# Performance work log

Hardware: AMD Instinct MI355X
Metric: run time of the kernel (lower is better)

The kernel has to match this reference:

```python
import jax, jax.numpy as jnp
import numpy as np

N_FREQ = 48  # tcnn Frequency encoding n_frequencies


def _freq_encode(x):
    # x: [N,3] in [0,1]; tcnn Frequency: sin/cos of x * 2^f * pi, f=0..F-1
    freqs = (2.0 ** jnp.arange(N_FREQ, dtype=jnp.float32)) * jnp.pi  # [F]
    ang = x[:, :, None] * freqs  # [N,3,F]
    enc = jnp.stack([jnp.sin(ang), jnp.cos(ang)], axis=-1)  # [N,3,F,2]
    return enc.reshape(x.shape[0], -1)  # [N, 3*F*2]


def _bilinear_sample(plane, coords):
    # plane: [R,R,F] (H,W,feat); coords: [N,2] in [-1,1], coords[:,0]->width(x), coords[:,1]->height(y)
    # matches torch grid_sample(align_corners=True, bilinear) for in-range coords
    R = plane.shape[0]
    gx = (coords[:, 0] + 1.0) * 0.5 * (R - 1)
    gy = (coords[:, 1] + 1.0) * 0.5 * (R - 1)
    x0f = jnp.clip(jnp.floor(gx), 0.0, R - 1)
    y0f = jnp.clip(jnp.floor(gy), 0.0, R - 1)
    x0 = x0f.astype(jnp.int32)
    y0 = y0f.astype(jnp.int32)
    x1 = jnp.minimum(x0 + 1, R - 1)
    y1 = jnp.minimum(y0 + 1, R - 1)
    wx = (gx - x0f)[:, None]
    wy = (gy - y0f)[:, None]
    v00 = plane[y0, x0]
    v01 = plane[y0, x1]
    v10 = plane[y1, x0]
    v11 = plane[y1, x1]
    return (v00 * (1 - wx) * (1 - wy) + v01 * wx * (1 - wy)
            + v10 * (1 - wx) * wy + v11 * wx * wy)  # [N,F]


def setup_inputs() -> dict:
    key = jax.random.key(0)
    ks = jax.random.split(key, 8)
    N = 524288
    res, fdim = 32, 16
    enc_dim = 3 * N_FREQ * 2  # 288
    d_in = enc_dim + fdim     # 304
    h = 64
    positions = jax.random.uniform(ks[0], (N, 3), dtype=jnp.float32)
    aabb = jnp.array([0.0, 0.0, 0.0, 1.0, 1.0, 1.0], dtype=jnp.float32)
    triplane = jax.random.normal(ks[1], (3, res, res, fdim), dtype=jnp.float32) * 0.001
    W0 = jax.random.normal(ks[2], (d_in, h), dtype=jnp.float32) / np.sqrt(d_in)
    W1 = jax.random.normal(ks[3], (h, h), dtype=jnp.float32) / np.sqrt(h)
    W2 = jax.random.normal(ks[4], (h, h), dtype=jnp.float32) / np.sqrt(h)
    W3 = jax.random.normal(ks[5], (h, 4), dtype=jnp.float32) / np.sqrt(h)
    return {"positions": positions, "aabb": aabb, "triplane": triplane,
            "W0": W0, "W1": W1, "W2": W2, "W3": W3}


def reference(positions, aabb, triplane, W0, W1, W2, W3):
    aabb_min, aabb_max = aabb[:3], aabb[3:]
    xn = (positions - aabb_min) / (aabb_max - aabb_min)          # normalized [0,1]
    sc = 2.0 * xn - 1.0                                          # scaled_coords in [-1,1]
    selector = jnp.all((xn > 0.0) & (xn < 1.0), axis=-1)
    # plane coordinate pairs as in the torch code
    coords = jnp.stack([
        jnp.stack([sc[:, 0], sc[:, 1]], axis=1),  # xy
        jnp.stack([sc[:, 0], sc[:, 2]], axis=1),  # xz
        jnp.stack([sc[:, 1], sc[:, 2]], axis=1),  # zy
    ], axis=0)  # [3,N,2]
    feats = jax.vmap(_bilinear_sample)(triplane, coords).sum(0)  # [N,fdim]
    h = jnp.concatenate([_freq_encode(xn), feats], axis=1)       # [N,304]
    h = jnp.sin(h @ W0)
    h = jnp.sin(h @ W1)
    h = jnp.sin(h @ W2)
    out = h @ W3                                                 # [N,4]
    rgb = jax.nn.sigmoid(out[:, :3])
    density = jnp.exp(out[:, 3:4] - 1.0) * selector[:, None]     # trunc_exp(x-1)
    return rgb, density
```

## Files before the change

kernel.cpp:

```cpp
#include <hip/hip_runtime.h>
#include <stdint.h>

typedef _Float16 half8  __attribute__((ext_vector_type(8)));
typedef _Float16 half2v __attribute__((ext_vector_type(2)));
typedef float f32x4 __attribute__((ext_vector_type(4)));

#define TPW 8
#define WPB 8
#define NT  512
#define W0S 304

__device__ __forceinline__ half2v pkrtz(float a, float b) {
    return __builtin_bit_cast(half2v, __builtin_amdgcn_cvt_pkrtz(a, b));
}

static __device__ __forceinline__ void wave_fence() {
    __builtin_amdgcn_wave_barrier();
    asm volatile("" ::: "memory");
}

__device__ __forceinline__ float bf2f(uint16_t u) {
    return __uint_as_float(((uint32_t)u) << 16);
}
__device__ __forceinline__ uint16_t f2bf(float f) {
    uint32_t u = __float_as_uint(f);
    u = (u + 0x7FFFu + ((u >> 16) & 1u)) >> 16;
    return (uint16_t)u;
}

template<bool BF>
__device__ __forceinline__ float lde(const void* p, uint32_t i) {
    if constexpr (BF) return bf2f(((const uint16_t*)p)[i]);
    else              return ((const float*)p)[i];
}
template<bool BF>
__device__ __forceinline__ void st1(void* p, uint32_t i, float v) {
    if constexpr (BF) ((uint16_t*)p)[i] = f2bf(v);
    else              ((float*)p)[i] = v;
}
template<bool BF>
__device__ __forceinline__ void ld8(const void* p, uint32_t i, float* o) {
    if constexpr (BF) {
        const uint4 c = *(const uint4*)((const uint16_t*)p + i);
        const uint32_t* pu = (const uint32_t*)&c;
#pragma unroll
        for (int j = 0; j < 4; ++j) {
            o[2 * j]     = __uint_as_float(pu[j] << 16);
            o[2 * j + 1] = __uint_as_float(pu[j] & 0xFFFF0000u);
        }
    } else {
        const float4 a = *(const float4*)((const float*)p + i);
        const float4 b = *(const float4*)((const float*)p + i + 4);
        o[0] = a.x; o[1] = a.y; o[2] = a.z; o[3] = a.w;
        o[4] = b.x; o[5] = b.y; o[6] = b.z; o[7] = b.w;
    }
}

__device__ __forceinline__ int hswz(int p, int g) {
    return p * 72 + ((g + 2 * (p >> 2)) & 7) * 8;
}

template<bool BF>
__device__ __forceinline__ void run_all(
    const void* __restrict__ posg, const void* __restrict__ aabbg,
    const void* __restrict__ tpg,
    const void* __restrict__ w0g, const void* __restrict__ w1g,
    const void* __restrict__ w2g, const void* __restrict__ w3g,
    void* __restrict__ outp, int npts,
    _Float16* w0t, _Float16* w1t, _Float16* w2t, _Float16* w3t, _Float16* hbuf)
{
    const int tid = threadIdx.x;
    const float I2PI = 0.15915494309189535f;

    for (int e = tid; e < 16; e += NT) w0t[64 * W0S + e] = (_Float16)0.0f;
    for (int e = tid; e < 304 * 64; e += NT) { int k = e >> 6, n = e & 63; w0t[n * W0S + k] = (_Float16)(lde<BF>(w0g, e) * I2PI); }
    for (int e = tid; e < 64 * 64;  e += NT) { int k = e >> 6, n = e & 63; w1t[n * 72 + k] = (_Float16)(lde<BF>(w1g, e) * I2PI);
                                               w2t[n * 72 + k] = (_Float16)(lde<BF>(w2g, e) * I2PI); }
    for (int e = tid; e < 64 * 4;   e += NT) { int k = e >> 2, n = e & 3;  w3t[n * 72 + k] = (_Float16)lde<BF>(w3g, e); }
    __syncthreads();

    const int w = tid >> 6, lane = tid & 63;
    const int m = lane & 15, q = lane >> 4;
    _Float16* hb = hbuf + w * (16 * 72);

    const float mn0 = lde<BF>(aabbg, 0), mn1 = lde<BF>(aabbg, 1), mn2 = lde<BF>(aabbg, 2);
    const float mx0 = lde<BF>(aabbg, 3), mx1 = lde<BF>(aabbg, 4), mx2 = lde<BF>(aabbg, 5);

    const double IH = 0x1.45f306dc9c883p-2;
    const double IL = -0x1.6b01ec5417056p-56;
    const float PIF  = 3.14159274101257324f;
    const f32x4 z4 = {0.f, 0.f, 0.f, 0.f};

    const int tile0 = (blockIdx.x * WPB + w) * TPW;

    float cp0, cp1, cp2;
    {
        const int pt = tile0 * 16 + m;
        cp0 = lde<BF>(posg, 3 * pt + 0);
        cp1 = lde<BF>(posg, 3 * pt + 1);
        cp2 = lde<BF>(posg, 3 * pt + 2);
    }

    for (int it = 0; it < TPW; ++it) {
        const int base = (tile0 + it) * 16;
        const float p0 = cp0, p1 = cp1, p2 = cp2;
        {
            const int nit = (it + 1 < TPW) ? it + 1 : it;
            const int pt2 = (tile0 + nit) * 16 + m;
            cp0 = lde<BF>(posg, 3 * pt2 + 0);
            cp1 = lde<BF>(posg, 3 * pt2 + 1);
            cp2 = lde<BF>(posg, 3 * pt2 + 2);
        }

        float xn[3];
        xn[0] = (p0 - mn0) / (mx0 - mn0);
        xn[1] = (p1 - mn1) / (mx1 - mn1);
        xn[2] = (p2 - mn2) / (mx2 - mn2);

        const bool sel = xn[0] > 0.f && xn[0] < 1.f && xn[1] > 0.f && xn[1] < 1.f
                      && xn[2] > 0.f && xn[2] < 1.f;
        const unsigned long long bm = __ballot(sel);

        double wh[3], wl[3];
#pragma unroll
        for (int d = 0; d < 3; ++d) {
            const float mf = xn[d] * PIF;
            const double md = (double)mf;
            const double hi = md * IH;
            const double r  = __builtin_fma(md, IH, -hi);
            wh[d] = hi;
            wl[d] = __builtin_fma(md, IL, r);
        }

        float fe[8];
#pragma unroll
        for (int j = 0; j < 8; ++j) fe[j] = 0.f;
        if (q < 2) {
            const int fo = q * 8;
            float g[3];
#pragma unroll
            for (int d = 0; d < 3; ++d) g[d] = xn[d] * 31.f;
            float v[8];
#pragma unroll
            for (int p = 0; p < 3; ++p) {
                const float gx = (p == 2) ? g[1] : g[0];
                const float gy = (p == 0) ? g[1] : g[2];
                const float x0f = fminf(fmaxf(floorf(gx), 0.f), 31.f);
                const float y0f = fminf(fmaxf(floorf(gy), 0.f), 31.f);
                const int x0 = (int)x0f, y0 = (int)y0f;
                int x1 = x0 + 1; if (x1 > 31) x1 = 31;
                int y1 = y0 + 1; if (y1 > 31) y1 = 31;
                const float wx = gx - x0f, wy = gy - y0f;
                const float w00 = (1.f - wx) * (1.f - wy);
                const float w01 = wx * (1.f - wy);
                const float w10 = (1.f - wx) * wy;
                const float w11 = wx * wy;
                const uint32_t pb = p * 16384 + fo;
                ld8<BF>(tpg, pb + y0 * 512 + x0 * 16, v);
#pragma unroll
                for (int j = 0; j < 8; ++j) fe[j] += v[j] * w00;
                ld8<BF>(tpg, pb + y0 * 512 + x1 * 16, v);
#pragma unroll
                for (int j = 0; j < 8; ++j) fe[j] += v[j] * w01;
                ld8<BF>(tpg, pb + y1 * 512 + x0 * 16, v);
#pragma unroll
                for (int j = 0; j < 8; ++j) fe[j] += v[j] * w10;
                ld8<BF>(tpg, pb + y1 * 512 + x1 * 16, v);
#pragma unroll
                for (int j = 0; j < 8; ++j) fe[j] += v[j] * w11;
            }
        }

        f32x4 acc[4] = {z4, z4, z4, z4};
#pragma unroll
        for (int d = 0; d < 3; ++d) {
#pragma unroll
            for (int cc = 0; cc < 3; ++cc) {
                const int e0 = 16 * cc + 4 * q - 1;
                const double zp = __builtin_bit_cast(double, (uint64_t)(1023 + e0) << 52);
                const double z  = wh[d] * zp;
                const double zl = wl[d] * zp;
                const double fr = z - __builtin_floor(z);
                const float t = (float)(fr + zl);
                float s = __builtin_amdgcn_sinf(t);
                float c = __builtin_amdgcn_cosf(t);
                union { half8 h8; half2v h2[4]; } au;
                au.h2[0] = pkrtz(s, c);
#pragma unroll
                for (int jj = 1; jj < 4; ++jj) {
                    const float t2 = s + s;
                    const float sn = t2 * c;
                    c = __builtin_fmaf(-t2, s, 1.0f);
                    s = sn;
                    au.h2[jj] = pkrtz(s, c);
                }
                const int ch = 3 * d + cc;
#pragma unroll
                for (int t4 = 0; t4 < 4; ++t4) {
                    const half8 b = *(const half8*)&w0t[(t4 * 16 + m) * W0S + ch * 32 + q * 8];
                    acc[t4] = __builtin_amdgcn_mfma_f32_16x16x32_f16(au.h8, b, acc[t4], 0, 0, 0);
                }
            }
        }
        {
            union { half8 h8; half2v h2[4]; } au;
            if (q < 2) {
#pragma unroll
                for (int i = 0; i < 4; ++i)
                    au.h2[i] = pkrtz(fe[2 * i], fe[2 * i + 1]);
            } else {
#pragma unroll
                for (int j = 0; j < 8; ++j) au.h8[j] = (_Float16)0.f;
            }
#pragma unroll
            for (int t4 = 0; t4 < 4; ++t4) {
                const half8 b = *(const half8*)&w0t[(t4 * 16 + m) * W0S + 288 + q * 8];
                acc[t4] = __builtin_amdgcn_mfma_f32_16x16x32_f16(au.h8, b, acc[t4], 0, 0, 0);
            }
        }

#pragma unroll
        for (int t4 = 0; t4 < 4; ++t4) {
            const int gw = 2 * t4 + (m >> 3);
#pragma unroll
            for (int rg = 0; rg < 4; ++rg)
                hb[hswz(4 * q + rg, gw) + (m & 7)] =
                    (_Float16)__builtin_amdgcn_sinf(acc[t4][rg]);
        }
        wave_fence();

        f32x4 acc2[4] = {z4, z4, z4, z4};
#pragma unroll
        for (int c = 0; c < 2; ++c) {
            const half8 a = *(const half8*)&hb[hswz(m, 4 * c + q)];
#pragma unroll
            for (int t4 = 0; t4 < 4; ++t4) {
                const half8 b = *(const half8*)&w1t[(t4 * 16 + m) * 72 + c * 32 + q * 8];
                acc2[t4] = __builtin_amdgcn_mfma_f32_16x16x32_f16(a, b, acc2[t4], 0, 0, 0);
            }
        }
        wave_fence();
#pragma unroll
        for (int t4 = 0; t4 < 4; ++t4) {
            const int gw = 2 * t4 + (m >> 3);
#pragma unroll
            for (int rg = 0; rg < 4; ++rg)
                hb[hswz(4 * q + rg, gw) + (m & 7)] =
                    (_Float16)__builtin_amdgcn_sinf(acc2[t4][rg]);
        }
        wave_fence();

        f32x4 accx[4] = {z4, z4, z4, z4};
#pragma unroll
        for (int c = 0; c < 2; ++c) {
            const half8 a = *(const half8*)&hb[hswz(m, 4 * c + q)];
#pragma unroll
            for (int t4 = 0; t4 < 4; ++t4) {
                const half8 b = *(const half8*)&w2t[(t4 * 16 + m) * 72 + c * 32 + q * 8];
                accx[t4] = __builtin_amdgcn_mfma_f32_16x16x32_f16(a, b, accx[t4], 0, 0, 0);
            }
        }
        wave_fence();
#pragma unroll
        for (int t4 = 0; t4 < 4; ++t4) {
            const int gw = 2 * t4 + (m >> 3);
#pragma unroll
            for (int rg = 0; rg < 4; ++rg)
                hb[hswz(4 * q + rg, gw) + (m & 7)] =
                    (_Float16)__builtin_amdgcn_sinf(accx[t4][rg]);
        }
        wave_fence();

        f32x4 acc3 = z4;
#pragma unroll
        for (int c = 0; c < 2; ++c) {
            const half8 a = *(const half8*)&hb[hswz(m, 4 * c + q)];
            const half8 b = *(const half8*)&w3t[(m & 3) * 72 + c * 32 + q * 8];
            acc3 = __builtin_amdgcn_mfma_f32_16x16x32_f16(a, b, acc3, 0, 0, 0);
        }
        wave_fence();

        if (m < 3) {
#pragma unroll
            for (int rg = 0; rg < 4; ++rg) {
                const float s = 1.f / (1.f + __expf(-acc3[rg]));
                st1<BF>(outp, (uint32_t)(base + 4 * q + rg) * 3u + m, s);
            }
        } else if (m == 3) {
            float dv[4];
#pragma unroll
            for (int rg = 0; rg < 4; ++rg) {
                float dens = __expf(acc3[rg] - 1.f);
                if (!((bm >> (4 * q + rg)) & 1ull)) dens = 0.f;
                dv[rg] = dens;
            }
            const uint32_t di = 3u * (uint32_t)npts + (uint32_t)(base + 4 * q);
            if constexpr (BF) {
                ushort4 pk;
                pk.x = f2bf(dv[0]); pk.y = f2bf(dv[1]);
                pk.z = f2bf(dv[2]); pk.w = f2bf(dv[3]);
                *(ushort4*)((uint16_t*)outp + di) = pk;
            } else {
                float4 pk = {dv[0], dv[1], dv[2], dv[3]};
                *(float4*)((float*)outp + di) = pk;
            }
        }
    }
}

__global__ __launch_bounds__(NT, 2)
void tri_mlp(const void* __restrict__ posg, const void* __restrict__ aabbg,
             const void* __restrict__ tpg,
             const void* __restrict__ w0g, const void* __restrict__ w1g,
             const void* __restrict__ w2g, const void* __restrict__ w3g,
             void* __restrict__ outp, int npts)
{
    __shared__ alignas(16) _Float16 w0t[64 * W0S + 16];
    __shared__ alignas(16) _Float16 w1t[64 * 72];
    __shared__ alignas(16) _Float16 w2t[64 * 72];
    __shared__ alignas(16) _Float16 w3t[4 * 72];
    __shared__ alignas(16) _Float16 hbuf[WPB * 16 * 72];

    const bool bf = (((const uint32_t*)aabbg)[2] != 0u);
    if (bf) run_all<true >(posg, aabbg, tpg, w0g, w1g, w2g, w3g, outp, npts, w0t, w1t, w2t, w3t, hbuf);
    else    run_all<false>(posg, aabbg, tpg, w0g, w1g, w2g, w3g, outp, npts, w0t, w1t, w2t, w3t, hbuf);
}

extern "C" void kernel_launch(void* const* d_in, const int* in_sizes, int n_in,
                              void* d_out, int out_size, void* d_ws, size_t ws_size,
                              hipStream_t stream) {
    const int npts = in_sizes[0] / 3;
    const int blocks = npts / (16 * WPB * TPW);
    tri_mlp<<<blocks, NT, 0, stream>>>(d_in[0], d_in[1], d_in[2], d_in[3],
                                       d_in[4], d_in[5], d_in[6], d_out, npts);
}
```

Measured before the change: 146.3 us.

## Swap MFMA operand roles and pass hidden activations via ds_bpermute instead of LDS

Transposes the MLP GEMMs so weights feed the A operand and activations the B operand, making each lane's accumulator hold a point's outputs. Hidden activations between layers are then re-laid out with cross-lane ds_bpermute shuffles instead of a per-wave LDS round trip with wave barriers, and the hbuf shared buffer is removed. This cuts LDS stores, loads and fences per layer and lowers shared memory use. The output stage now writes per point from q==0 lanes using the local selector instead of a ballot. In exchange it adds bpermute traffic and some register pressure.

New measurement: 280.9 us. +91.9%, slower.

```diff
diff --git a/kernel.cpp b/kernel.cpp
--- a/kernel.cpp
+++ b/kernel.cpp
@@ -12,11 +12,6 @@
 
 __device__ __forceinline__ half2v pkrtz(float a, float b) {
     return __builtin_bit_cast(half2v, __builtin_amdgcn_cvt_pkrtz(a, b));
-}
-
-static __device__ __forceinline__ void wave_fence() {
-    __builtin_amdgcn_wave_barrier();
-    asm volatile("" ::: "memory");
 }
 
 __device__ __forceinline__ float bf2f(uint16_t u) {
@@ -56,8 +51,30 @@
     }
 }
 
-__device__ __forceinline__ int hswz(int p, int g) {
-    return p * 72 + ((g + 2 * (p >> 2)) & 7) * 8;
+__device__ __forceinline__ void sin_shuffle(const f32x4* acc, int addr0, bool hi,
+                                            half8* b0, half8* b1) {
+    uint32_t P[8];
+#pragma unroll
+    for (int t4 = 0; t4 < 4; ++t4) {
+        const float s0 = __builtin_amdgcn_sinf(acc[t4][0]);
+        const float s1 = __builtin_amdgcn_sinf(acc[t4][1]);
+        const float s2 = __builtin_amdgcn_sinf(acc[t4][2]);
+        const float s3 = __builtin_amdgcn_sinf(acc[t4][3]);
+        P[2 * t4]     = __builtin_bit_cast(uint32_t, pkrtz(s0, s1));
+        P[2 * t4 + 1] = __builtin_bit_cast(uint32_t, pkrtz(s2, s3));
+    }
+    union { uint32_t d[4]; half8 h8; } u0, u1;
+#pragma unroll
+    for (int c = 0; c < 2; ++c) {
+#pragma unroll
+        for (int jd = 0; jd < 4; ++jd) {
+            const int ad = addr0 + (jd >> 1) * 64;
+            const uint32_t lo = (uint32_t)__builtin_amdgcn_ds_bpermute(ad, (int)P[4 * c + (jd & 1)]);
+            const uint32_t hv = (uint32_t)__builtin_amdgcn_ds_bpermute(ad, (int)P[4 * c + 2 + (jd & 1)]);
+            (c ? u1.d : u0.d)[jd] = hi ? hv : lo;
+        }
+    }
+    *b0 = u0.h8; *b1 = u1.h8;
 }
 
 template<bool BF>
@@ -67,7 +84,7 @@
     const void* __restrict__ w0g, const void* __restrict__ w1g,
     const void* __restrict__ w2g, const void* __restrict__ w3g,
     void* __restrict__ outp, int npts,
-    _Float16* w0t, _Float16* w1t, _Float16* w2t, _Float16* w3t, _Float16* hbuf)
+    _Float16* w0t, _Float16* w1t, _Float16* w2t, _Float16* w3t)
 {
     const int tid = threadIdx.x;
     const float I2PI = 0.15915494309189535f;
@@ -81,7 +98,8 @@
 
     const int w = tid >> 6, lane = tid & 63;
     const int m = lane & 15, q = lane >> 4;
-    _Float16* hb = hbuf + w * (16 * 72);
+    const int addr0 = (m + 32 * (q & 1)) * 4;
+    const bool hi = (q >> 1) != 0;
 
     const float mn0 = lde<BF>(aabbg, 0), mn1 = lde<BF>(aabbg, 1), mn2 = lde<BF>(aabbg, 2);
     const float mx0 = lde<BF>(aabbg, 3), mx1 = lde<BF>(aabbg, 4), mx2 = lde<BF>(aabbg, 5);
@@ -119,16 +137,15 @@
 
         const bool sel = xn[0] > 0.f && xn[0] < 1.f && xn[1] > 0.f && xn[1] < 1.f
                       && xn[2] > 0.f && xn[2] < 1.f;
-        const unsigned long long bm = __ballot(sel);
 
         double wh[3], wl[3];
 #pragma unroll
         for (int d = 0; d < 3; ++d) {
             const float mf = xn[d] * PIF;
             const double md = (double)mf;
-            const double hi = md * IH;
-            const double r  = __builtin_fma(md, IH, -hi);
-            wh[d] = hi;
+            const double hid = md * IH;
+            const double r  = __builtin_fma(md, IH, -hid);
+            wh[d] = hid;
             wl[d] = __builtin_fma(md, IL, r);
         }
 
@@ -197,8 +214,8 @@
                 const int ch = 3 * d + cc;
 #pragma unroll
                 for (int t4 = 0; t4 < 4; ++t4) {
-                    const half8 b = *(const half8*)&w0t[(t4 * 16 + m) * W0S + ch * 32 + q * 8];
-                    acc[t4] = __builtin_amdgcn_mfma_f32_16x16x32_f16(au.h8, b, acc[t4], 0, 0, 0);
+                    const half8 aw = *(const half8*)&w0t[(t4 * 16 + m) * W0S + ch * 32 + q * 8];
+                    acc[t4] = __builtin_amdgcn_mfma_f32_16x16x32_f16(aw, au.h8, acc[t4], 0, 0, 0);
                 }
             }
         }
@@ -214,96 +231,54 @@
             }
 #pragma unroll
             for (int t4 = 0; t4 < 4; ++t4) {
-                const half8 b = *(const half8*)&w0t[(t4 * 16 + m) * W0S + 288 + q * 8];
-                acc[t4] = __builtin_amdgcn_mfma_f32_16x16x32_f16(au.h8, b, acc[t4], 0, 0, 0);
-            }
-        }
-
-#pragma unroll
-        for (int t4 = 0; t4 < 4; ++t4) {
-            const int gw = 2 * t4 + (m >> 3);
-#pragma unroll
-            for (int rg = 0; rg < 4; ++rg)
-                hb[hswz(4 * q + rg, gw) + (m & 7)] =
-                    (_Float16)__builtin_amdgcn_sinf(acc[t4][rg]);
-        }
-        wave_fence();
-
+                const half8 aw = *(const half8*)&w0t[(t4 * 16 + m) * W0S + 288 + q * 8];
+                acc[t4] = __builtin_amdgcn_mfma_f32_16x16x32_f16(aw, au.h8, acc[t4], 0, 0, 0);
+            }
+        }
+
+        half8 hb0, hb1;
+        sin_shuffle(acc, addr0, hi, &hb0, &hb1);
         f32x4 acc2[4] = {z4, z4, z4, z4};
 #pragma unroll
         for (int c = 0; c < 2; ++c) {
-            const half8 a = *(const half8*)&hb[hswz(m, 4 * c + q)];
+            const half8 bfr = c ? hb1 : hb0;
 #pragma unroll
             for (int t4 = 0; t4 < 4; ++t4) {
-                const half8 b = *(const half8*)&w1t[(t4 * 16 + m) * 72 + c * 32 + q * 8];
-                acc2[t4] = __builtin_amdgcn_mfma_f32_16x16x32_f16(a, b, acc2[t4], 0, 0, 0);
-            }
-        }
-        wave_fence();
-#pragma unroll
-        for (int t4 = 0; t4 < 4; ++t4) {
-            const int gw = 2 * t4 + (m >> 3);
-#pragma unroll
-            for (int rg = 0; rg < 4; ++rg)
-                hb[hswz(4 * q + rg, gw) + (m & 7)] =
-                    (_Float16)__builtin_amdgcn_sinf(acc2[t4][rg]);
-        }
-        wave_fence();
-
+                const half8 aw = *(const half8*)&w1t[(t4 * 16 + m) * 72 + c * 32 + q * 8];
+                acc2[t4] = __builtin_amdgcn_mfma_f32_16x16x32_f16(aw, bfr, acc2[t4], 0, 0, 0);
+            }
+        }
+
+        sin_shuffle(acc2, addr0, hi, &hb0, &hb1);
         f32x4 accx[4] = {z4, z4, z4, z4};
 #pragma unroll
         for (int c = 0; c < 2; ++c) {
-            const half8 a = *(const half8*)&hb[hswz(m, 4 * c + q)];
+            const half8 bfr = c ? hb1 : hb0;
 #pragma unroll
             for (int t4 = 0; t4 < 4; ++t4) {
-                const half8 b = *(const half8*)&w2t[(t4 * 16 + m) * 72 + c * 32 + q * 8];
-                accx[t4] = __builtin_amdgcn_mfma_f32_16x16x32_f16(a, b, accx[t4], 0, 0, 0);
-            }
-        }
-        wave_fence();
-#pragma unroll
-        for (int t4 = 0; t4 < 4; ++t4) {
-            const int gw = 2 * t4 + (m >> 3);
-#pragma unroll
-            for (int rg = 0; rg < 4; ++rg)
-                hb[hswz(4 * q + rg, gw) + (m & 7)] =
-                    (_Float16)__builtin_amdgcn_sinf(accx[t4][rg]);
-        }
-        wave_fence();
-
+                const half8 aw = *(const half8*)&w2t[(t4 * 16 + m) * 72 + c * 32 + q * 8];
+                accx[t4] = __builtin_amdgcn_mfma_f32_16x16x32_f16(aw, bfr, accx[t4], 0, 0, 0);
+            }
+        }
+
+        sin_shuffle(accx, addr0, hi, &hb0, &hb1);
         f32x4 acc3 = z4;
 #pragma unroll
         for (int c = 0; c < 2; ++c) {
-            const half8 a = *(const half8*)&hb[hswz(m, 4 * c + q)];
-            const half8 b = *(const half8*)&w3t[(m & 3) * 72 + c * 32 + q * 8];
-            acc3 = __builtin_amdgcn_mfma_f32_16x16x32_f16(a, b, acc3, 0, 0, 0);
-        }
-        wave_fence();
-
-        if (m < 3) {
-#pragma unroll
-            for (int rg = 0; rg < 4; ++rg) {
-                const float s = 1.f / (1.f + __expf(-acc3[rg]));
-                st1<BF>(outp, (uint32_t)(base + 4 * q + rg) * 3u + m, s);
-            }
-        } else if (m == 3) {
-            float dv[4];
-#pragma unroll
-            for (int rg = 0; rg < 4; ++rg) {
-                float dens = __expf(acc3[rg] - 1.f);
-                if (!((bm >> (4 * q + rg)) & 1ull)) dens = 0.f;
-                dv[rg] = dens;
-            }
-            const uint32_t di = 3u * (uint32_t)npts + (uint32_t)(base + 4 * q);
-            if constexpr (BF) {
-                ushort4 pk;
-                pk.x = f2bf(dv[0]); pk.y = f2bf(dv[1]);
-                pk.z = f2bf(dv[2]); pk.w = f2bf(dv[3]);
-                *(ushort4*)((uint16_t*)outp + di) = pk;
-            } else {
-                float4 pk = {dv[0], dv[1], dv[2], dv[3]};
-                *(float4*)((float*)outp + di) = pk;
-            }
+            const half8 bfr = c ? hb1 : hb0;
+            const half8 aw = *(const half8*)&w3t[(m & 3) * 72 + c * 32 + q * 8];
+            acc3 = __builtin_amdgcn_mfma_f32_16x16x32_f16(aw, bfr, acc3, 0, 0, 0);
+        }
+
+        if (q == 0) {
+#pragma unroll
+            for (int c = 0; c < 3; ++c) {
+                const float s = 1.f / (1.f + __expf(-acc3[c]));
+                st1<BF>(outp, (uint32_t)(base + m) * 3u + c, s);
+            }
+            float dens = __expf(acc3[3] - 1.f);
+            if (!sel) dens = 0.f;
+            st1<BF>(outp, 3u * (uint32_t)npts + (uint32_t)(base + m), dens);
         }
     }
 }
@@ -319,11 +294,10 @@
     __shared__ alignas(16) _Float16 w1t[64 * 72];
     __shared__ alignas(16) _Float16 w2t[64 * 72];
     __shared__ alignas(16) _Float16 w3t[4 * 72];
-    __shared__ alignas(16) _Float16 hbuf[WPB * 16 * 72];
 
     const bool bf = (((const uint32_t*)aabbg)[2] != 0u);
-    if (bf) run_all<true >(posg, aabbg, tpg, w0g, w1g, w2g, w3g, outp, npts, w0t, w1t, w2t, w3t, hbuf);
-    else    run_all<false>(posg, aabbg, tpg, w0g, w1g, w2g, w3g, outp, npts, w0t, w1t, w2t, w3t, hbuf);
+    if (bf) run_all<true >(posg, aabbg, tpg, w0g, w1g, w2g, w3g, outp, npts, w0t, w1t, w2t, w3t);
+    else    run_all<false>(posg, aabbg, tpg, w0g, w1g, w2g, w3g, outp, npts, w0t, w1t, w2t, w3t);
 }
 
 extern "C" void kernel_launch(void* const* d_in, const int* in_sizes, int n_in,
```

## Process two 16-point tiles per iteration to interleave MFMA chains

Applied to the files above, without the earlier changes.

Each wave now handles two tiles per loop iteration. The encoding, triplane sampling and first-layer MFMAs for both tiles are interleaved so the two independent accumulator chains can hide MFMA latency, and the weight-fragment LDS reads are shared between the tiles. The hidden layers are staggered per tile through the single per-wave scratch buffer. The wave_barrier builtin is dropped and only a compiler memory fence is kept. This roughly doubles accumulator register pressure, which could cause spills or lower occupancy at launch bounds (512,2), and leaves LDS ordering within the wave resting on the compiler fence alone.

Measured after the change: 150.2 us. 2.6% more time.

```diff
diff --git a/kernel.cpp b/kernel.cpp
--- a/kernel.cpp
+++ b/kernel.cpp
@@ -14,8 +14,7 @@
     return __builtin_bit_cast(half2v, __builtin_amdgcn_cvt_pkrtz(a, b));
 }
 
-static __device__ __forceinline__ void wave_fence() {
-    __builtin_amdgcn_wave_barrier();
+static __device__ __forceinline__ void mem_fence() {
     asm volatile("" ::: "memory");
 }
 
@@ -93,216 +92,230 @@
 
     const int tile0 = (blockIdx.x * WPB + w) * TPW;
 
-    float cp0, cp1, cp2;
-    {
-        const int pt = tile0 * 16 + m;
-        cp0 = lde<BF>(posg, 3 * pt + 0);
-        cp1 = lde<BF>(posg, 3 * pt + 1);
-        cp2 = lde<BF>(posg, 3 * pt + 2);
+    auto xpose_sin = [&](const f32x4* a4) {
+#pragma unroll
+        for (int t4 = 0; t4 < 4; ++t4) {
+            const int gw = 2 * t4 + (m >> 3);
+#pragma unroll
+            for (int rg = 0; rg < 4; ++rg)
+                hb[hswz(4 * q + rg, gw) + (m & 7)] =
+                    (_Float16)__builtin_amdgcn_sinf(a4[t4][rg]);
+        }
+    };
+    auto hidden = [&](const _Float16* wt, f32x4* out) {
+#pragma unroll
+        for (int t4 = 0; t4 < 4; ++t4) out[t4] = z4;
+#pragma unroll
+        for (int c = 0; c < 2; ++c) {
+            const half8 a = *(const half8*)&hb[hswz(m, 4 * c + q)];
+#pragma unroll
+            for (int t4 = 0; t4 < 4; ++t4) {
+                const half8 b = *(const half8*)&wt[(t4 * 16 + m) * 72 + c * 32 + q * 8];
+                out[t4] = __builtin_amdgcn_mfma_f32_16x16x32_f16(a, b, out[t4], 0, 0, 0);
+            }
+        }
+    };
+
+    float cp[2][3];
+#pragma unroll
+    for (int t = 0; t < 2; ++t) {
+        const int pt = (tile0 + t) * 16 + m;
+        cp[t][0] = lde<BF>(posg, 3 * pt + 0);
+        cp[t][1] = lde<BF>(posg, 3 * pt + 1);
+        cp[t][2] = lde<BF>(posg, 3 * pt + 2);
     }
 
-    for (int it = 0; it < TPW; ++it) {
-        const int base = (tile0 + it) * 16;
-        const float p0 = cp0, p1 = cp1, p2 = cp2;
+    for (int io = 0; io < TPW / 2; ++io) {
+        const int baseA = (tile0 + 2 * io) * 16;
+        float pp[2][3];
+#pragma unroll
+        for (int t = 0; t < 2; ++t) {
+            pp[t][0] = cp[t][0]; pp[t][1] = cp[t][1]; pp[t][2] = cp[t][2];
+        }
         {
-            const int nit = (it + 1 < TPW) ? it + 1 : it;
-            const int pt2 = (tile0 + nit) * 16 + m;
-            cp0 = lde<BF>(posg, 3 * pt2 + 0);
-            cp1 = lde<BF>(posg, 3 * pt2 + 1);
-            cp2 = lde<BF>(posg, 3 * pt2 + 2);
-        }
-
-        float xn[3];
-        xn[0] = (p0 - mn0) / (mx0 - mn0);
-        xn[1] = (p1 - mn1) / (mx1 - mn1);
-        xn[2] = (p2 - mn2) / (mx2 - mn2);
-
-        const bool sel = xn[0] > 0.f && xn[0] < 1.f && xn[1] > 0.f && xn[1] < 1.f
-                      && xn[2] > 0.f && xn[2] < 1.f;
-        const unsigned long long bm = __ballot(sel);
-
-        double wh[3], wl[3];
-#pragma unroll
-        for (int d = 0; d < 3; ++d) {
-            const float mf = xn[d] * PIF;
-            const double md = (double)mf;
-            const double hi = md * IH;
-            const double r  = __builtin_fma(md, IH, -hi);
-            wh[d] = hi;
-            wl[d] = __builtin_fma(md, IL, r);
-        }
-
-        float fe[8];
-#pragma unroll
-        for (int j = 0; j < 8; ++j) fe[j] = 0.f;
-        if (q < 2) {
-            const int fo = q * 8;
-            float g[3];
-#pragma unroll
-            for (int d = 0; d < 3; ++d) g[d] = xn[d] * 31.f;
-            float v[8];
-#pragma unroll
-            for (int p = 0; p < 3; ++p) {
-                const float gx = (p == 2) ? g[1] : g[0];
-                const float gy = (p == 0) ? g[1] : g[2];
-                const float x0f = fminf(fmaxf(floorf(gx), 0.f), 31.f);
-                const float y0f = fminf(fmaxf(floorf(gy), 0.f), 31.f);
-                const int x0 = (int)x0f, y0 = (int)y0f;
-                int x1 = x0 + 1; if (x1 > 31) x1 = 31;
-                int y1 = y0 + 1; if (y1 > 31) y1 = 31;
-                const float wx = gx - x0f, wy = gy - y0f;
-                const float w00 = (1.f - wx) * (1.f - wy);
-                const float w01 = wx * (1.f - wy);
-                const float w10 = (1.f - wx) * wy;
-                const float w11 = wx * wy;
-                const uint32_t pb = p * 16384 + fo;
-                ld8<BF>(tpg, pb + y0 * 512 + x0 * 16, v);
-#pragma unroll
-                for (int j = 0; j < 8; ++j) fe[j] += v[j] * w00;
-                ld8<BF>(tpg, pb + y0 * 512 + x1 * 16, v);
-#pragma unroll
-                for (int j = 0; j < 8; ++j) fe[j] += v[j] * w01;
-                ld8<BF>(tpg, pb + y1 * 512 + x0 * 16, v);
-#pragma unroll
-                for (int j = 0; j < 8; ++j) fe[j] += v[j] * w10;
-                ld8<BF>(tpg, pb + y1 * 512 + x1 * 16, v);
-#pragma unroll
-                for (int j = 0; j < 8; ++j) fe[j] += v[j] * w11;
-            }
-        }
-
-        f32x4 acc[4] = {z4, z4, z4, z4};
+            const int nio = (io + 1 < TPW / 2) ? io + 1 : io;
+#pragma unroll
+            for (int t = 0; t < 2; ++t) {
+                const int pt2 = (tile0 + 2 * nio + t) * 16 + m;
+                cp[t][0] = lde<BF>(posg, 3 * pt2 + 0);
+                cp[t][1] = lde<BF>(posg, 3 * pt2 + 1);
+                cp[t][2] = lde<BF>(posg, 3 * pt2 + 2);
+            }
+        }
+
+        bool sel[2];
+        double wh[2][3], wl[2][3];
+        float fe[2][8];
+#pragma unroll
+        for (int t = 0; t < 2; ++t) {
+            float xn[3];
+            xn[0] = (pp[t][0] - mn0) / (mx0 - mn0);
+            xn[1] = (pp[t][1] - mn1) / (mx1 - mn1);
+            xn[2] = (pp[t][2] - mn2) / (mx2 - mn2);
+            sel[t] = xn[0] > 0.f && xn[0] < 1.f && xn[1] > 0.f && xn[1] < 1.f
+                  && xn[2] > 0.f && xn[2] < 1.f;
+#pragma unroll
+            for (int d = 0; d < 3; ++d) {
+                const float mf = xn[d] * PIF;
+                const double md = (double)mf;
+                const double hi = md * IH;
+                const double r  = __builtin_fma(md, IH, -hi);
+                wh[t][d] = hi;
+                wl[t][d] = __builtin_fma(md, IL, r);
+            }
+#pragma unroll
+            for (int j = 0; j < 8; ++j) fe[t][j] = 0.f;
+            if (q < 2) {
+                const int fo = q * 8;
+                float g[3];
+#pragma unroll
+                for (int d = 0; d < 3; ++d) g[d] = xn[d] * 31.f;
+                float v[8];
+#pragma unroll
+                for (int p = 0; p < 3; ++p) {
+                    const float gx = (p == 2) ? g[1] : g[0];
+                    const float gy = (p == 0) ? g[1] : g[2];
+                    const float x0f = fminf(fmaxf(floorf(gx), 0.f), 31.f);
+                    const float y0f = fminf(fmaxf(floorf(gy), 0.f), 31.f);
+                    const int x0 = (int)x0f, y0 = (int)y0f;
+                    int x1 = x0 + 1; if (x1 > 31) x1 = 31;
+                    int y1 = y0 + 1; if (y1 > 31) y1 = 31;
+                    const float wx = gx - x0f, wy = gy - y0f;
+                    const float w00 = (1.f - wx) * (1.f - wy);
+                    const float w01 = wx * (1.f - wy);
+                    const float w10 = (1.f - wx) * wy;
+                    const float w11 = wx * wy;
+                    const uint32_t pb = p * 16384 + fo;
+                    ld8<BF>(tpg, pb + y0 * 512 + x0 * 16, v);
+#pragma unroll
+                    for (int j = 0; j < 8; ++j) fe[t][j] += v[j] * w00;
+                    ld8<BF>(tpg, pb + y0 * 512 + x1 * 16, v);
+#pragma unroll
+                    for (int j = 0; j < 8; ++j) fe[t][j] += v[j] * w01;
+                    ld8<BF>(tpg, pb + y1 * 512 + x0 * 16, v);
+#pragma unroll
+                    for (int j = 0; j < 8; ++j) fe[t][j] += v[j] * w10;
+                    ld8<BF>(tpg, pb + y1 * 512 + x1 * 16, v);
+#pragma unroll
+                    for (int j = 0; j < 8; ++j) fe[t][j] += v[j] * w11;
+                }
+            }
+        }
+
+        f32x4 acc0[2][4];
+#pragma unroll
+        for (int t = 0; t < 2; ++t)
+#pragma unroll
+            for (int t4 = 0; t4 < 4; ++t4) acc0[t][t4] = z4;
+
+        {
+            half8 au[2];
+#pragma unroll
+            for (int t = 0; t < 2; ++t) {
+                union { half8 h8; half2v h2[4]; } u;
+                if (q < 2) {
+#pragma unroll
+                    for (int i = 0; i < 4; ++i)
+                        u.h2[i] = pkrtz(fe[t][2 * i], fe[t][2 * i + 1]);
+                } else {
+#pragma unroll
+                    for (int j = 0; j < 8; ++j) u.h8[j] = (_Float16)0.f;
+                }
+                au[t] = u.h8;
+            }
+#pragma unroll
+            for (int t4 = 0; t4 < 4; ++t4) {
+                const half8 b = *(const half8*)&w0t[(t4 * 16 + m) * W0S + 288 + q * 8];
+                acc0[0][t4] = __builtin_amdgcn_mfma_f32_16x16x32_f16(au[0], b, acc0[0][t4], 0, 0, 0);
+                acc0[1][t4] = __builtin_amdgcn_mfma_f32_16x16x32_f16(au[1], b, acc0[1][t4], 0, 0, 0);
+            }
+        }
 #pragma unroll
         for (int d = 0; d < 3; ++d) {
 #pragma unroll
             for (int cc = 0; cc < 3; ++cc) {
                 const int e0 = 16 * cc + 4 * q - 1;
                 const double zp = __builtin_bit_cast(double, (uint64_t)(1023 + e0) << 52);
-                const double z  = wh[d] * zp;
-                const double zl = wl[d] * zp;
-                const double fr = z - __builtin_floor(z);
-                const float t = (float)(fr + zl);
-                float s = __builtin_amdgcn_sinf(t);
-                float c = __builtin_amdgcn_cosf(t);
-                union { half8 h8; half2v h2[4]; } au;
-                au.h2[0] = pkrtz(s, c);
-#pragma unroll
-                for (int jj = 1; jj < 4; ++jj) {
-                    const float t2 = s + s;
-                    const float sn = t2 * c;
-                    c = __builtin_fmaf(-t2, s, 1.0f);
-                    s = sn;
-                    au.h2[jj] = pkrtz(s, c);
+                half8 au[2];
+#pragma unroll
+                for (int t = 0; t < 2; ++t) {
+                    const double z  = wh[t][d] * zp;
+                    const double zl = wl[t][d] * zp;
+                    const double fr = z - __builtin_floor(z);
+                    const float tv = (float)(fr + zl);
+                    float s = __builtin_amdgcn_sinf(tv);
+                    float c = __builtin_amdgcn_cosf(tv);
+                    union { half8 h8; half2v h2[4]; } u;
+                    u.h2[0] = pkrtz(s, c);
+#pragma unroll
+                    for (int jj = 1; jj < 4; ++jj) {
+                        const float t2 = s + s;
+                        const float sn = t2 * c;
+                        c = __builtin_fmaf(-t2, s, 1.0f);
+                        s = sn;
+                        u.h2[jj] = pkrtz(s, c);
+                    }
+                    au[t] = u.h8;
                 }
                 const int ch = 3 * d + cc;
 #pragma unroll
                 for (int t4 = 0; t4 < 4; ++t4) {
                     const half8 b = *(const half8*)&w0t[(t4 * 16 + m) * W0S + ch * 32 + q * 8];
-                    acc[t4] = __builtin_amdgcn_mfma_f32_16x16x32_f16(au.h8, b, acc[t4], 0, 0, 0);
-                }
-            }
-        }
-        {
-            union { half8 h8; half2v h2[4]; } au;
-            if (q < 2) {
-#pragma unroll
-                for (int i = 0; i < 4; ++i)
-                    au.h2[i] = pkrtz(fe[2 * i], fe[2 * i + 1]);
-            } else {
-#pragma unroll
-                for (int j = 0; j < 8; ++j) au.h8[j] = (_Float16)0.f;
-            }
-#pragma unroll
-            for (int t4 = 0; t4 < 4; ++t4) {
-                const half8 b = *(const half8*)&w0t[(t4 * 16 + m) * W0S + 288 + q * 8];
-                acc[t4] = __builtin_amdgcn_mfma_f32_16x16x32_f16(au.h8, b, acc[t4], 0, 0, 0);
-            }
-        }
-
-#pragma unroll
-        for (int t4 = 0; t4 < 4; ++t4) {
-            const int gw = 2 * t4 + (m >> 3);
-#pragma unroll
-            for (int rg = 0; rg < 4; ++rg)
-                hb[hswz(4 * q + rg, gw) + (m & 7)] =
-                    (_Float16)__builtin_amdgcn_sinf(acc[t4][rg]);
-        }
-        wave_fence();
-
-        f32x4 acc2[4] = {z4, z4, z4, z4};
-#pragma unroll
-        for (int c = 0; c < 2; ++c) {
-            const half8 a = *(const half8*)&hb[hswz(m, 4 * c + q)];
-#pragma unroll
-            for (int t4 = 0; t4 < 4; ++t4) {
-                const half8 b = *(const half8*)&w1t[(t4 * 16 + m) * 72 + c * 32 + q * 8];
-                acc2[t4] = __builtin_amdgcn_mfma_f32_16x16x32_f16(a, b, acc2[t4], 0, 0, 0);
-            }
-        }
-        wave_fence();
-#pragma unroll
-        for (int t4 = 0; t4 < 4; ++t4) {
-            const int gw = 2 * t4 + (m >> 3);
-#pragma unroll
-            for (int rg = 0; rg < 4; ++rg)
-                hb[hswz(4 * q + rg, gw) + (m & 7)] =
-                    (_Float16)__builtin_amdgcn_sinf(acc2[t4][rg]);
-        }
-        wave_fence();
-
-        f32x4 accx[4] = {z4, z4, z4, z4};
-#pragma unroll
-        for (int c = 0; c < 2; ++c) {
-            const half8 a = *(const half8*)&hb[hswz(m, 4 * c + q)];
-#pragma unroll
-            for (int t4 = 0; t4 < 4; ++t4) {
-                const half8 b = *(const half8*)&w2t[(t4 * 16 + m) * 72 + c * 32 + q * 8];
-                accx[t4] = __builtin_amdgcn_mfma_f32_16x16x32_f16(a, b, accx[t4], 0, 0, 0);
-            }
-        }
-        wave_fence();
-#pragma unroll
-        for (int t4 = 0; t4 < 4; ++t4) {
-            const int gw = 2 * t4 + (m >> 3);
-#pragma unroll
-            for (int rg = 0; rg < 4; ++rg)
-                hb[hswz(4 * q + rg, gw) + (m & 7)] =
-                    (_Float16)__builtin_amdgcn_sinf(accx[t4][rg]);
-        }
-        wave_fence();
-
-        f32x4 acc3 = z4;
-#pragma unroll
-        for (int c = 0; c < 2; ++c) {
-            const half8 a = *(const half8*)&hb[hswz(m, 4 * c + q)];
-            const half8 b = *(const half8*)&w3t[(m & 3) * 72 + c * 32 + q * 8];
-            acc3 = __builtin_amdgcn_mfma_f32_16x16x32_f16(a, b, acc3, 0, 0, 0);
-        }
-        wave_fence();
-
-        if (m < 3) {
-#pragma unroll
-            for (int rg = 0; rg < 4; ++rg) {
-                const float s = 1.f / (1.f + __expf(-acc3[rg]));
-                st1<BF>(outp, (uint32_t)(base + 4 * q + rg) * 3u + m, s);
-            }
-        } else if (m == 3) {
-            float dv[4];
-#pragma unroll
-            for (int rg = 0; rg < 4; ++rg) {
-                float dens = __expf(acc3[rg] - 1.f);
-                if (!((bm >> (4 * q + rg)) & 1ull)) dens = 0.f;
-                dv[rg] = dens;
-            }
-            const uint32_t di = 3u * (uint32_t)npts + (uint32_t)(base + 4 * q);
-            if constexpr (BF) {
-                ushort4 pk;
-                pk.x = f2bf(dv[0]); pk.y = f2bf(dv[1]);
-                pk.z = f2bf(dv[2]); pk.w = f2bf(dv[3]);
-                *(ushort4*)((uint16_t*)outp + di) = pk;
-            } else {
-                float4 pk = {dv[0], dv[1], dv[2], dv[3]};
-                *(float4*)((float*)outp + di) = pk;
+                    acc0[0][t4] = __builtin_amdgcn_mfma_f32_16x16x32_f16(au[0], b, acc0[0][t4], 0, 0, 0);
+                    acc0[1][t4] = __builtin_amdgcn_mfma_f32_16x16x32_f16(au[1], b, acc0[1][t4], 0, 0, 0);
+                }
+            }
+        }
+
+        f32x4 h1[2][4], h2[2][4];
+#pragma unroll
+        for (int t = 0; t < 2; ++t) {
+            xpose_sin(acc0[t]);  mem_fence();
+            hidden(w1t, h1[t]);  mem_fence();
+        }
+#pragma unroll
+        for (int t = 0; t < 2; ++t) {
+            xpose_sin(h1[t]);    mem_fence();
+            hidden(w2t, h2[t]);  mem_fence();
+        }
+#pragma unroll
+        for (int t = 0; t < 2; ++t) {
+            xpose_sin(h2[t]);    mem_fence();
+            f32x4 acc3 = z4;
+#pragma unroll
+            for (int c = 0; c < 2; ++c) {
+                const half8 a = *(const half8*)&hb[hswz(m, 4 * c + q)];
+                const half8 b = *(const half8*)&w3t[(m & 3) * 72 + c * 32 + q * 8];
+                acc3 = __builtin_amdgcn_mfma_f32_16x16x32_f16(a, b, acc3, 0, 0, 0);
+            }
+            mem_fence();
+
+            const int base = baseA + 16 * t;
+            const unsigned long long bm = __ballot(sel[t]);
+            if (m < 3) {
+#pragma unroll
+                for (int rg = 0; rg < 4; ++rg) {
+                    const float s = 1.f / (1.f + __expf(-acc3[rg]));
+                    st1<BF>(outp, (uint32_t)(base + 4 * q + rg) * 3u + m, s);
+                }
+            } else if (m == 3) {
+                float dv[4];
+#pragma unroll
+                for (int rg = 0; rg < 4; ++rg) {
+                    float dens = __expf(acc3[rg] - 1.f);
+                    if (!((bm >> (4 * q + rg)) & 1ull)) dens = 0.f;
+                    dv[rg] = dens;
+                }
+                const uint32_t di = 3u * (uint32_t)npts + (uint32_t)(base + 4 * q);
+                if constexpr (BF) {
+                    ushort4 pk;
+                    pk.x = f2bf(dv[0]); pk.y = f2bf(dv[1]);
+                    pk.z = f2bf(dv[2]); pk.w = f2bf(dv[3]);
+                    *(ushort4*)((uint16_t*)outp + di) = pk;
+                } else {
+                    float4 pk = {dv[0], dv[1], dv[2], dv[3]};
+                    *(float4*)((float*)outp + di) = pk;
+                }
             }
         }
     }
```
